# Kernel optimization log

Hardware: AMD Instinct MI355X
Metric: run time of the kernel (lower is better)

The kernel has to match this reference:

```python
import jax, jax.numpy as jnp
import numpy as np
import itertools, math

METRIC = [1.0, 1.0, 1.0]  # Cl(3,0)
EPS = 1e-6
SQRT2 = math.sqrt(2.0)


def _build_algebra(metric):
    d = len(metric)
    # basis blades ordered by grade, then lexicographic combination (repo convention)
    blades = []
    for g in range(d + 1):
        for c in itertools.combinations(range(d), g):
            blades.append(sum(1 << i for i in c))
    idx = {m: i for i, m in enumerate(blades)}
    n = len(blades)
    C = np.zeros((n, n, n), dtype=np.float32)  # cayley[i, j, k]: e_i * e_k -> sign * e_j
    for ia, am in enumerate(blades):
        for ik, bm in enumerate(blades):
            a = am >> 1
            swaps = 0
            while a:
                swaps += bin(a & bm).count('1')
                a >>= 1
            sign = -1.0 if (swaps & 1) else 1.0
            for i in range(d):
                if am & bm & (1 << i):
                    sign *= metric[i]
            C[ia, idx[am ^ bm], ik] = sign
    grades = np.array([bin(m).count('1') for m in blades])
    subspaces = np.array([int((grades == g).sum()) for g in range(d + 1)])
    paths = np.zeros((d + 1, d + 1, d + 1), dtype=bool)
    for i in range(d + 1):
        for j in range(d + 1):
            for k in range(d + 1):
                paths[i, j, k] = np.any(C[np.ix_(grades == i, grades == j, grades == k)] != 0)
    return C, subspaces, paths, grades

CAYLEY_NP, SUBSPACES, PATHS, GRADE_OF_COMP = _build_algebra(METRIC)
REP_IDX = np.repeat(np.arange(len(SUBSPACES)), SUBSPACES)  # component -> grade, len 8
PI, PJ, PK = np.nonzero(PATHS)                              # 20 active grade triples
ONEHOT_GRADE = np.eye(len(SUBSPACES), dtype=np.float32)[GRADE_OF_COMP]  # [8,4]

B, N_IN, N_OUT = 1024, 256, 256
DIM_MV = CAYLEY_NP.shape[0]  # 8
N_PATHS = int(PATHS.sum())   # 20


def mv_linear(x, w, bias=None):
    # MVLinear: per-grade weight repeated over components; einsum 'bm...i,nmi->bn...i'
    wr = w[:, :, REP_IDX]                       # [out, in, 8]
    out = jnp.einsum('bmi,nmi->bni', x, wr)
    if bias is not None:
        out = out.at[:, :, 0].add(bias[:, :, 0])  # bias embedded in scalar (grade-0) slot
    return out


def normalize_mv(x, a):
    # per-grade norms (Euclidean metric => L2 norm of each grade block)
    oh = jnp.asarray(ONEHOT_GRADE)
    norms = jnp.sqrt(jnp.einsum('bni,ig->bng', x * x, oh))  # [b, n, 4]
    interp = jax.nn.sigmoid(a)[None] * (norms - 1.0) + 1.0  # learned interp toward unit norm
    return x / (interp[:, :, REP_IDX] + EPS)


def gp_kernel(gp_weight):
    # scatter 20 path weights into (m, n, 4, 4, 4), repeat per subspace, mask by cayley
    m, n, _ = gp_weight.shape
    g = len(SUBSPACES)
    w4 = jnp.zeros((m, n, g, g, g), gp_weight.dtype).at[:, :, PI, PJ, PK].set(gp_weight)
    wrep = w4[:, :, REP_IDX][:, :, :, REP_IDX][:, :, :, :, REP_IDX]  # [m, n, 8, 8, 8]
    return jnp.asarray(CAYLEY_NP)[None, None] * wrep


def setup_inputs() -> dict:
    key = jax.random.key(0)
    ks = jax.random.split(key, 5)
    std_gp = 1.0 / math.sqrt(N_IN * (len(METRIC) + 1))
    std_lin = 1.0 / math.sqrt(N_IN)
    return {
        'x': jax.random.normal(ks[0], (B, N_IN, DIM_MV), jnp.float32),
        'w_right': jax.random.normal(ks[1], (N_IN, N_IN, len(SUBSPACES)), jnp.float32) * std_lin,
        'w_left': jax.random.normal(ks[2], (N_OUT, N_IN, len(SUBSPACES)), jnp.float32) * std_lin,
        'b_left': jax.random.normal(ks[3], (1, N_OUT, 1), jnp.float32) * 0.02,
        'norm_a': jnp.zeros((N_IN, len(SUBSPACES)), jnp.float32),  # normalization_init = 0
        'gp_weight': jax.random.normal(ks[4], (N_OUT, N_IN, N_PATHS), jnp.float32) * std_gp,
    }


def reference(x, w_right, w_left, b_left, norm_a, gp_weight):
    x_right = normalize_mv(mv_linear(x, w_right), norm_a)
    kernel = gp_kernel(gp_weight)                 # [m, n, 8, 8, 8]
    outer = jnp.einsum('bni,bnk->bnik', x, x_right)  # [b, n, 8, 8]
    prod = jnp.einsum('bnik,mnijk->bmj', outer, kernel)
    left = mv_linear(x, w_left, b_left)
    return (left + prod) / SQRT2
```

## Files before the change

### kernel.cpp

```cpp
#include <hip/hip_runtime.h>
#include <math.h>

typedef unsigned short ushortT;
typedef __bf16 bf16x8 __attribute__((ext_vector_type(8)));
typedef float  f32x4  __attribute__((ext_vector_type(4)));

__constant__ int GRADEc[8] = {0,1,1,1,2,2,2,3};

__constant__ int CMAPc[8][7] = {
  {0, 8, 9,10,11, 0, 0},
  {1,12,13,14,15,16,17},
  {2,18,19,20,21,22,23},
  {3,24,25,26,27,28,29},
  {4,30,31,32,33,34,35},
  {5,36,37,38,39,40,41},
  {6,42,43,44,45,46,47},
  {7,48,49,50,51, 0, 0}};
__constant__ int WMAPc[8][7] = {
  {0, 4, 8,14,20, 0, 0},
  {1, 5, 9,10,15,16,21},
  {1, 5, 9,10,15,16,21},
  {1, 5, 9,10,15,16,21},
  {2, 6,11,12,17,18,22},
  {2, 6,11,12,17,18,22},
  {2, 6,11,12,17,18,22},
  {3, 7,13,19,23, 0, 0}};
__constant__ int SSTARTc[8][4] = {
  {0,2,3,4},{0,2,4,6},{0,2,4,6},{0,2,4,6},
  {0,2,4,6},{0,2,4,6},{0,2,4,6},{0,2,3,4}};
__constant__ int SCOUNTc[8][4] = {
  {2,1,1,1},{2,2,2,1},{2,2,2,1},{2,2,2,1},
  {2,2,2,1},{2,2,2,1},{2,2,2,1},{2,1,1,1}};

__device__ __forceinline__ ushortT f2bf(float f) {
  unsigned int u = __float_as_uint(f);
  unsigned int r = (u + 0x7fffu + ((u >> 16) & 1u)) >> 16;
  return (ushortT)r;
}

#define GLOAD_LDS16(gsrc, ldst) \
  __builtin_amdgcn_global_load_lds((const __attribute__((address_space(1))) unsigned int*)(gsrc), \
                                   (__attribute__((address_space(3))) unsigned int*)(ldst), 16, 0, 0)

__global__ void k_xsplit(const float* __restrict__ x, ushortT* __restrict__ XH,
                         ushortT* __restrict__ XL) {
  const int b = blockIdx.x;
  const int m = threadIdx.x;
  const float4* xp = (const float4*)(x + b * 2048 + m * 8);
  float4 a = xp[0], c = xp[1];
  float v[8] = {a.x, a.y, a.z, a.w, c.x, c.y, c.z, c.w};
  #pragma unroll
  for (int i = 0; i < 8; ++i) {
    ushortT h = f2bf(v[i]);
    float hf = __uint_as_float(((unsigned int)h) << 16);
    XH[i * 262144 + b * 256 + m] = h;
    XL[i * 262144 + b * 256 + m] = f2bf(v[i] - hf);
  }
}

__global__ void k_wsplit(const float* __restrict__ w_right, ushortT* __restrict__ WH,
                         ushortT* __restrict__ WL) {
  const int n = blockIdx.x;
  const int m = threadIdx.x;
  float4 w = *(const float4*)(w_right + n * 1024 + m * 4);
  float v[4] = {w.x, w.y, w.z, w.w};
  #pragma unroll
  for (int g = 0; g < 4; ++g) {
    ushortT h = f2bf(v[g]);
    float hf = __uint_as_float(((unsigned int)h) << 16);
    WH[g * 65536 + n * 256 + m] = h;
    WL[g * 65536 + n * 256 + m] = f2bf(v[g] - hf);
  }
}

__global__ void k_build_wt2(const float* __restrict__ w_left, const float* __restrict__ gp,
                            ushortT* __restrict__ WT2b) {
  int t = blockIdx.x * 256 + threadIdx.x;
  int n = t & 255, m = (t >> 8) & 255, w = t >> 16;
  float v;
  if (w < 4)       v = w_left[m * 1024 + n * 4 + w];
  else             v = gp[m * 5120 + n * 20 + (w - 4)];
  WT2b[t] = f2bf(v);
}

__global__ __launch_bounds__(256) void k_right_mfma(const ushortT* __restrict__ XH,
                                                    const ushortT* __restrict__ XL,
                                                    const ushortT* __restrict__ WH,
                                                    const ushortT* __restrict__ WL,
                                                    float* __restrict__ y2) {
  const int i  = blockIdx.z;
  const int g  = GRADEc[i];
  const int b0 = blockIdx.y * 64;
  const int n0 = blockIdx.x * 64;
  __shared__ __align__(16) ushortT lds[4 * 2048];
  const int t = threadIdx.x;
  const int wave = t >> 6, lane = t & 63;
  const int wb = (wave & 1) * 32, wn = (wave >> 1) * 32;
  const int lrow = lane & 15, lkg = lane >> 4;

  const ushortT* Ah = XH + i * 262144 + b0 * 256;
  const ushortT* Al = XL + i * 262144 + b0 * 256;
  const ushortT* Bh = WH + g * 65536 + n0 * 256;
  const ushortT* Bl = WL + g * 65536 + n0 * 256;
  const ushortT* gp0 = (wave == 0) ? Ah : (wave == 1) ? Al : (wave == 2) ? Bh : Bl;
  ushortT* lbase = lds + wave * 2048;

  const int srow = lane >> 2;
  const int sseg = lane & 3;

  f32x4 acc[2][2];
  #pragma unroll
  for (int r = 0; r < 2; ++r)
    #pragma unroll
    for (int c = 0; c < 2; ++c)
      acc[r][c] = (f32x4){0.f, 0.f, 0.f, 0.f};

  for (int k0 = 0; k0 < 256; k0 += 32) {
    #pragma unroll
    for (int q = 0; q < 4; ++q) {
      int row = q * 16 + srow;
      int slog = sseg ^ ((row >> 1) & 3);
      GLOAD_LDS16(gp0 + row * 256 + k0 + slog * 8, lbase + q * 512);
    }
    __syncthreads();
    bf16x8 afh[2], afl[2], bfh[2], bfl[2];
    #pragma unroll
    for (int r = 0; r < 2; ++r) {
      int row = wb + r * 16 + lrow;
      int po = row * 32 + (lkg ^ ((row >> 1) & 3)) * 8;
      afh[r] = *(const bf16x8*)(lds + po);
      afl[r] = *(const bf16x8*)(lds + 2048 + po);
    }
    #pragma unroll
    for (int c = 0; c < 2; ++c) {
      int row = wn + c * 16 + lrow;
      int po = row * 32 + (lkg ^ ((row >> 1) & 3)) * 8;
      bfh[c] = *(const bf16x8*)(lds + 4096 + po);
      bfl[c] = *(const bf16x8*)(lds + 6144 + po);
    }
    #pragma unroll
    for (int r = 0; r < 2; ++r)
      #pragma unroll
      for (int c = 0; c < 2; ++c) {
        acc[r][c] = __builtin_amdgcn_mfma_f32_16x16x32_bf16(afh[r], bfh[c], acc[r][c], 0, 0, 0);
        acc[r][c] = __builtin_amdgcn_mfma_f32_16x16x32_bf16(afl[r], bfh[c], acc[r][c], 0, 0, 0);
        acc[r][c] = __builtin_amdgcn_mfma_f32_16x16x32_bf16(afh[r], bfl[c], acc[r][c], 0, 0, 0);
      }
    __syncthreads();
  }

  #pragma unroll
  for (int r = 0; r < 2; ++r)
    #pragma unroll
    for (int c = 0; c < 2; ++c)
      #pragma unroll
      for (int e = 0; e < 4; ++e) {
        int brow = b0 + wb + r * 16 + lkg * 4 + e;
        int ncol = n0 + wn + c * 16 + lrow;
        y2[i * 262144 + brow * 256 + ncol] = acc[r][c][e];
      }
}

__global__ void k_features2(const float* __restrict__ y2, const float* __restrict__ x,
                            const float* __restrict__ norm_a, ushortT* __restrict__ FT2b) {
  const int b = blockIdx.x;
  const int n = threadIdx.x;
  float y[8], xv[8];
  #pragma unroll
  for (int i = 0; i < 8; ++i) y[i] = y2[i * 262144 + b * 256 + n];
  const float4* xp = (const float4*)(x + b * 2048 + n * 8);
  float4 x01 = xp[0], x23 = xp[1];
  xv[0]=x01.x; xv[1]=x01.y; xv[2]=x01.z; xv[3]=x01.w;
  xv[4]=x23.x; xv[5]=x23.y; xv[6]=x23.z; xv[7]=x23.w;
  float4 na = *(const float4*)(norm_a + n * 4);
  float nav[4] = {na.x, na.y, na.z, na.w};
  float nr[4];
  nr[0] = fabsf(y[0]);
  nr[1] = sqrtf(y[1]*y[1] + y[2]*y[2] + y[3]*y[3]);
  nr[2] = sqrtf(y[4]*y[4] + y[5]*y[5] + y[6]*y[6]);
  nr[3] = fabsf(y[7]);
  float inv[4];
  #pragma unroll
  for (int g = 0; g < 4; ++g) {
    float s = 1.0f / (1.0f + expf(-nav[g]));
    inv[g] = 1.0f / (s * (nr[g] - 1.0f) + 1.0f + 1e-6f);
  }
  float r[8];
  r[0] = y[0]*inv[0];
  r[1] = y[1]*inv[1]; r[2] = y[2]*inv[1]; r[3] = y[3]*inv[1];
  r[4] = y[4]*inv[2]; r[5] = y[5]*inv[2]; r[6] = y[6]*inv[2];
  r[7] = y[7]*inv[3];

  float F[52];
  F[8]  = xv[0]*r[0];
  F[9]  = xv[1]*r[1] + xv[2]*r[2] + xv[3]*r[3];
  F[10] = -(xv[4]*r[4] + xv[5]*r[5] + xv[6]*r[6]);
  F[11] = -xv[7]*r[7];
  F[12] = xv[0]*r[1];
  F[13] = xv[1]*r[0];
  F[14] = -(xv[2]*r[4] + xv[3]*r[5]);
  F[15] = xv[4]*r[2] + xv[5]*r[3];
  F[16] = -xv[6]*r[7];
  F[17] = -xv[7]*r[6];
  F[18] = xv[0]*r[2];
  F[19] = xv[2]*r[0];
  F[20] = xv[1]*r[4] - xv[3]*r[6];
  F[21] = -xv[4]*r[1] + xv[6]*r[3];
  F[22] = xv[5]*r[7];
  F[23] = xv[7]*r[5];
  F[24] = xv[0]*r[3];
  F[25] = xv[3]*r[0];
  F[26] = xv[1]*r[5] + xv[2]*r[6];
  F[27] = -(xv[5]*r[1] + xv[6]*r[2]);
  F[28] = -xv[4]*r[7];
  F[29] = -xv[7]*r[4];
  F[30] = xv[0]*r[4];
  F[31] = xv[1]*r[2] - xv[2]*r[1];
  F[32] = xv[3]*r[7];
  F[33] = xv[4]*r[0];
  F[34] = -xv[5]*r[6] + xv[6]*r[5];
  F[35] = xv[7]*r[3];
  F[36] = xv[0]*r[5];
  F[37] = xv[1]*r[3] - xv[3]*r[1];
  F[38] = -xv[2]*r[7];
  F[39] = xv[5]*r[0];
  F[40] = xv[4]*r[6] - xv[6]*r[4];
  F[41] = -xv[7]*r[2];
  F[42] = xv[0]*r[6];
  F[43] = xv[2]*r[3] - xv[3]*r[2];
  F[44] = xv[1]*r[7];
  F[45] = xv[6]*r[0];
  F[46] = -xv[4]*r[5] + xv[5]*r[4];
  F[47] = xv[7]*r[1];
  F[48] = xv[0]*r[7];
  F[49] = xv[1]*r[6] - xv[2]*r[5] + xv[3]*r[4];
  F[50] = xv[4]*r[3] - xv[5]*r[2] + xv[6]*r[1];
  F[51] = xv[7]*r[0];

  #pragma unroll
  for (int c = 8; c < 52; ++c)
    FT2b[c * 262144 + b * 256 + n] = f2bf(F[c]);
}

__global__ __launch_bounds__(256) void k_gemm_mfma(const ushortT* __restrict__ XH,
                                                   const ushortT* __restrict__ FT2b,
                                                   const ushortT* __restrict__ WT2b,
                                                   float* __restrict__ outP) {
  const int j  = blockIdx.z >> 2;
  const int ks = blockIdx.z & 3;
  const int b0 = blockIdx.y * 128;
  const int m0 = blockIdx.x * 128;
  __shared__ __align__(16) ushortT sA[128 * 64];
  __shared__ __align__(16) ushortT sB[128 * 64];
  const int t    = threadIdx.x;
  const int wave = t >> 6;
  const int lane = t & 63;
  const int wb   = (wave & 1) * 64;
  const int wm   = (wave >> 1) * 64;
  const int lrow = lane & 15;
  const int lkg  = lane >> 4;
  const int srow = lane >> 3;
  const int sseg = lane & 7;

  f32x4 acc[4][4];
  #pragma unroll
  for (int r = 0; r < 4; ++r)
    #pragma unroll
    for (int c = 0; c < 4; ++c)
      acc[r][c] = (f32x4){0.f, 0.f, 0.f, 0.f};

  const int sstart = SSTARTc[j][ks];
  const int scnt   = SCOUNTc[j][ks];
  for (int s2 = 0; s2 < scnt; ++s2) {
    const int slot = sstart + s2;
    const ushortT* Ap = ((slot == 0) ? (XH + j * 262144)
                                     : (FT2b + CMAPc[j][slot] * 262144)) + b0 * 256;
    const ushortT* Bp = WT2b + WMAPc[j][slot] * 65536 + m0 * 256;
    for (int k0 = 0; k0 < 256; k0 += 64) {
      #pragma unroll
      for (int q = 0; q < 4; ++q) {
        int idx = wave * 4 + q;
        int row = idx * 8 + srow;
        int slog = sseg ^ (row & 7);
        GLOAD_LDS16(Ap + row * 256 + k0 + slog * 8, sA + idx * 512);
        GLOAD_LDS16(Bp + row * 256 + k0 + slog * 8, sB + idx * 512);
      }
      __syncthreads();
      #pragma unroll
      for (int kk = 0; kk < 2; ++kk) {
        bf16x8 af[4], bf[4];
        #pragma unroll
        for (int r = 0; r < 4; ++r) {
          int row = wb + r * 16 + lrow;
          af[r] = *(const bf16x8*)(sA + row * 64 + (((kk * 4 + lkg) ^ (row & 7)) * 8));
        }
        #pragma unroll
        for (int c = 0; c < 4; ++c) {
          int row = wm + c * 16 + lrow;
          bf[c] = *(const bf16x8*)(sB + row * 64 + (((kk * 4 + lkg) ^ (row & 7)) * 8));
        }
        #pragma unroll
        for (int r = 0; r < 4; ++r)
          #pragma unroll
          for (int c = 0; c < 4; ++c)
            acc[r][c] = __builtin_amdgcn_mfma_f32_16x16x32_bf16(af[r], bf[c], acc[r][c], 0, 0, 0);
      }
      __syncthreads();
    }
  }

  float* oj = outP + (ks * 8 + j) * 262144;
  #pragma unroll
  for (int r = 0; r < 4; ++r) {
    #pragma unroll
    for (int c = 0; c < 4; ++c) {
      #pragma unroll
      for (int e = 0; e < 4; ++e) {
        int brow = b0 + wb + r * 16 + lkg * 4 + e;
        int mcol = m0 + wm + c * 16 + lrow;
        oj[brow * 256 + mcol] = acc[r][c][e];
      }
    }
  }
}

__global__ void k_merge(const float* __restrict__ outP, const float* __restrict__ bleft,
                        float* __restrict__ out) {
  const int idx = blockIdx.x * 256 + threadIdx.x;
  const int m = idx & 255;
  const float bias = bleft[m];
  const float sc = 0.7071067811865475f;
  float o[8];
  #pragma unroll
  for (int jj = 0; jj < 8; ++jj) {
    float s = 0.0f;
    #pragma unroll
    for (int p = 0; p < 4; ++p)
      s += outP[(p * 8 + jj) * 262144 + idx];
    o[jj] = s;
  }
  o[0] += bias;
  float4 v0 = make_float4(o[0]*sc, o[1]*sc, o[2]*sc, o[3]*sc);
  float4 v1 = make_float4(o[4]*sc, o[5]*sc, o[6]*sc, o[7]*sc);
  *(float4*)(out + idx * 8)     = v0;
  *(float4*)(out + idx * 8 + 4) = v1;
}

extern "C" void kernel_launch(void* const* d_in, const int* in_sizes, int n_in,
                              void* d_out, int out_size, void* d_ws, size_t ws_size,
                              hipStream_t stream) {
  const float* x       = (const float*)d_in[0];
  const float* w_right = (const float*)d_in[1];
  const float* w_left  = (const float*)d_in[2];
  const float* b_left  = (const float*)d_in[3];
  const float* norm_a  = (const float*)d_in[4];
  const float* gp      = (const float*)d_in[5];
  float* out = (float*)d_out;
  float* W   = (float*)d_ws;

  float*   y2   = W;
  float*   outP = W + 2097152;
  ushortT* XH   = (ushortT*)(W + 10485760);
  ushortT* XL   = (ushortT*)(W + 11534336);
  ushortT* WH   = (ushortT*)(W + 12582912);
  ushortT* WL   = (ushortT*)(W + 12713984);
  ushortT* FT2b = (ushortT*)(W + 12845056);
  ushortT* WT2b = (ushortT*)(W + 19660800);

  k_xsplit<<<1024, 256, 0, stream>>>(x, XH, XL);
  k_wsplit<<<256, 256, 0, stream>>>(w_right, WH, WL);
  k_build_wt2<<<6144, 256, 0, stream>>>(w_left, gp, WT2b);
  k_right_mfma<<<dim3(4, 16, 8), 256, 0, stream>>>(XH, XL, WH, WL, y2);
  k_features2<<<1024, 256, 0, stream>>>(y2, x, norm_a, FT2b);
  k_gemm_mfma<<<dim3(2, 8, 32), 256, 0, stream>>>(XH, FT2b, WT2b, outP);
  k_merge<<<1024, 256, 0, stream>>>(outP, b_left, out);
}
```

Baseline: 121.0 us.

## Fuse prep kernels, fuse right GEMM with features, double-buffer GEMM loads

The three conversion kernels are merged into one launch. The right-side bf16x3 GEMM and the feature construction are fused through LDS, which removes the y2 round trip to global memory. Both MFMA GEMMs now double-buffer LDS so global-to-LDS loads overlap the MFMA work. The merge kernel is vectorised with float4 loads. Together these cut launch count and memory traffic, at the cost of more LDS per block and smaller 32x32 tiles in the fused kernel, which may lower occupancy or increase redundant B loads.

```diff
diff --git a/kernel.cpp b/kernel.cpp
--- a/kernel.cpp
+++ b/kernel.cpp
@@ -42,72 +42,68 @@
   __builtin_amdgcn_global_load_lds((const __attribute__((address_space(1))) unsigned int*)(gsrc), \
                                    (__attribute__((address_space(3))) unsigned int*)(ldst), 16, 0, 0)
 
-__global__ void k_xsplit(const float* __restrict__ x, ushortT* __restrict__ XH,
-                         ushortT* __restrict__ XL) {
-  const int b = blockIdx.x;
-  const int m = threadIdx.x;
-  const float4* xp = (const float4*)(x + b * 2048 + m * 8);
-  float4 a = xp[0], c = xp[1];
-  float v[8] = {a.x, a.y, a.z, a.w, c.x, c.y, c.z, c.w};
-  #pragma unroll
-  for (int i = 0; i < 8; ++i) {
-    ushortT h = f2bf(v[i]);
-    float hf = __uint_as_float(((unsigned int)h) << 16);
-    XH[i * 262144 + b * 256 + m] = h;
-    XL[i * 262144 + b * 256 + m] = f2bf(v[i] - hf);
-  }
-}
-
-__global__ void k_wsplit(const float* __restrict__ w_right, ushortT* __restrict__ WH,
-                         ushortT* __restrict__ WL) {
-  const int n = blockIdx.x;
-  const int m = threadIdx.x;
-  float4 w = *(const float4*)(w_right + n * 1024 + m * 4);
-  float v[4] = {w.x, w.y, w.z, w.w};
-  #pragma unroll
-  for (int g = 0; g < 4; ++g) {
-    ushortT h = f2bf(v[g]);
-    float hf = __uint_as_float(((unsigned int)h) << 16);
-    WH[g * 65536 + n * 256 + m] = h;
-    WL[g * 65536 + n * 256 + m] = f2bf(v[g] - hf);
-  }
-}
-
-__global__ void k_build_wt2(const float* __restrict__ w_left, const float* __restrict__ gp,
-                            ushortT* __restrict__ WT2b) {
-  int t = blockIdx.x * 256 + threadIdx.x;
-  int n = t & 255, m = (t >> 8) & 255, w = t >> 16;
-  float v;
-  if (w < 4)       v = w_left[m * 1024 + n * 4 + w];
-  else             v = gp[m * 5120 + n * 20 + (w - 4)];
-  WT2b[t] = f2bf(v);
-}
-
-__global__ __launch_bounds__(256) void k_right_mfma(const ushortT* __restrict__ XH,
+__global__ void k_prep(const float* __restrict__ x, const float* __restrict__ w_right,
+                       const float* __restrict__ w_left, const float* __restrict__ gp,
+                       ushortT* __restrict__ XH, ushortT* __restrict__ XL,
+                       ushortT* __restrict__ WH, ushortT* __restrict__ WL,
+                       ushortT* __restrict__ WT2b) {
+  const int bid = blockIdx.x;
+  const int tid = threadIdx.x;
+  if (bid < 6144) {
+    int t = bid * 256 + tid;
+    int n = t & 255, m = (t >> 8) & 255, w = t >> 16;
+    float v = (w < 4) ? w_left[m * 1024 + n * 4 + w] : gp[m * 5120 + n * 20 + (w - 4)];
+    WT2b[t] = f2bf(v);
+  } else if (bid < 7168) {
+    int b = bid - 6144;
+    const float4* xp = (const float4*)(x + b * 2048 + tid * 8);
+    float4 a = xp[0], c = xp[1];
+    float v[8] = {a.x, a.y, a.z, a.w, c.x, c.y, c.z, c.w};
+    #pragma unroll
+    for (int i = 0; i < 8; ++i) {
+      ushortT h = f2bf(v[i]);
+      float hf = __uint_as_float(((unsigned int)h) << 16);
+      XH[i * 262144 + b * 256 + tid] = h;
+      XL[i * 262144 + b * 256 + tid] = f2bf(v[i] - hf);
+    }
+  } else {
+    int n = bid - 7168;
+    float4 w = *(const float4*)(w_right + n * 1024 + tid * 4);
+    float v[4] = {w.x, w.y, w.z, w.w};
+    #pragma unroll
+    for (int g = 0; g < 4; ++g) {
+      ushortT h = f2bf(v[g]);
+      float hf = __uint_as_float(((unsigned int)h) << 16);
+      WH[g * 65536 + n * 256 + tid] = h;
+      WL[g * 65536 + n * 256 + tid] = f2bf(v[g] - hf);
+    }
+  }
+}
+
+__global__ __launch_bounds__(512) void k_right_feat(const ushortT* __restrict__ XH,
                                                     const ushortT* __restrict__ XL,
                                                     const ushortT* __restrict__ WH,
                                                     const ushortT* __restrict__ WL,
-                                                    float* __restrict__ y2) {
-  const int i  = blockIdx.z;
-  const int g  = GRADEc[i];
-  const int b0 = blockIdx.y * 64;
-  const int n0 = blockIdx.x * 64;
-  __shared__ __align__(16) ushortT lds[4 * 2048];
-  const int t = threadIdx.x;
-  const int wave = t >> 6, lane = t & 63;
-  const int wb = (wave & 1) * 32, wn = (wave >> 1) * 32;
+                                                    const float* __restrict__ x,
+                                                    const float* __restrict__ norm_a,
+                                                    ushortT* __restrict__ FT2b) {
+  const int n0 = blockIdx.x * 32;
+  const int b0 = blockIdx.y * 32;
+  __shared__ __align__(16) ushortT lds[49152];
+  const int t    = threadIdx.x;
+  const int wave = t >> 6;
+  const int lane = t & 63;
+  const int i    = wave;
+  const int g    = GRADEc[i];
   const int lrow = lane & 15, lkg = lane >> 4;
-
-  const ushortT* Ah = XH + i * 262144 + b0 * 256;
-  const ushortT* Al = XL + i * 262144 + b0 * 256;
-  const ushortT* Bh = WH + g * 65536 + n0 * 256;
-  const ushortT* Bl = WL + g * 65536 + n0 * 256;
-  const ushortT* gp0 = (wave == 0) ? Ah : (wave == 1) ? Al : (wave == 2) ? Bh : Bl;
-  ushortT* lbase = lds + wave * 2048;
-
   const int srow = lane >> 2;
   const int sseg = lane & 3;
 
+  const ushortT* Asrc_h = XH + i * 262144 + b0 * 256;
+  const ushortT* Asrc_l = XL + i * 262144 + b0 * 256;
+  const int bg = wave >> 1;
+  const ushortT* Bsrc = ((wave & 1) ? WL : WH) + bg * 65536 + n0 * 256;
+
   f32x4 acc[2][2];
   #pragma unroll
   for (int r = 0; r < 2; ++r)
@@ -115,28 +111,35 @@
     for (int c = 0; c < 2; ++c)
       acc[r][c] = (f32x4){0.f, 0.f, 0.f, 0.f};
 
-  for (int k0 = 0; k0 < 256; k0 += 32) {
-    #pragma unroll
-    for (int q = 0; q < 4; ++q) {
+  auto STAGE = [&](int k0, int buf) {
+    ushortT* base = lds + buf * 24576;
+    #pragma unroll
+    for (int q = 0; q < 2; ++q) {
       int row = q * 16 + srow;
       int slog = sseg ^ ((row >> 1) & 3);
-      GLOAD_LDS16(gp0 + row * 256 + k0 + slog * 8, lbase + q * 512);
-    }
-    __syncthreads();
+      GLOAD_LDS16(Asrc_h + row * 256 + k0 + slog * 8, base + i * 1024 + q * 512);
+      GLOAD_LDS16(Asrc_l + row * 256 + k0 + slog * 8, base + 8192 + i * 1024 + q * 512);
+      GLOAD_LDS16(Bsrc   + row * 256 + k0 + slog * 8,
+                  base + 16384 + (wave & 1) * 4096 + bg * 1024 + q * 512);
+    }
+  };
+
+  auto COMPUTE = [&](int buf) {
+    const ushortT* base = lds + buf * 24576;
     bf16x8 afh[2], afl[2], bfh[2], bfl[2];
     #pragma unroll
     for (int r = 0; r < 2; ++r) {
-      int row = wb + r * 16 + lrow;
+      int row = r * 16 + lrow;
       int po = row * 32 + (lkg ^ ((row >> 1) & 3)) * 8;
-      afh[r] = *(const bf16x8*)(lds + po);
-      afl[r] = *(const bf16x8*)(lds + 2048 + po);
+      afh[r] = *(const bf16x8*)(base + i * 1024 + po);
+      afl[r] = *(const bf16x8*)(base + 8192 + i * 1024 + po);
     }
     #pragma unroll
     for (int c = 0; c < 2; ++c) {
-      int row = wn + c * 16 + lrow;
+      int row = c * 16 + lrow;
       int po = row * 32 + (lkg ^ ((row >> 1) & 3)) * 8;
-      bfh[c] = *(const bf16x8*)(lds + 4096 + po);
-      bfl[c] = *(const bf16x8*)(lds + 6144 + po);
+      bfh[c] = *(const bf16x8*)(base + 16384 + g * 1024 + po);
+      bfl[c] = *(const bf16x8*)(base + 20480 + g * 1024 + po);
     }
     #pragma unroll
     for (int r = 0; r < 2; ++r)
@@ -146,100 +149,111 @@
         acc[r][c] = __builtin_amdgcn_mfma_f32_16x16x32_bf16(afl[r], bfh[c], acc[r][c], 0, 0, 0);
         acc[r][c] = __builtin_amdgcn_mfma_f32_16x16x32_bf16(afh[r], bfl[c], acc[r][c], 0, 0, 0);
       }
+  };
+
+  STAGE(0, 0);
+  __syncthreads();
+  int cur = 0;
+  for (int tc = 0; tc < 8; ++tc) {
+    if (tc < 7) STAGE((tc + 1) * 32, cur ^ 1);
+    COMPUTE(cur);
     __syncthreads();
-  }
-
+    cur ^= 1;
+  }
+
+  float* yl = (float*)lds;
   #pragma unroll
   for (int r = 0; r < 2; ++r)
     #pragma unroll
     for (int c = 0; c < 2; ++c)
       #pragma unroll
       for (int e = 0; e < 4; ++e) {
-        int brow = b0 + wb + r * 16 + lkg * 4 + e;
-        int ncol = n0 + wn + c * 16 + lrow;
-        y2[i * 262144 + brow * 256 + ncol] = acc[r][c][e];
+        int row = r * 16 + lkg * 4 + e;
+        int col = c * 16 + lrow;
+        yl[i * 1056 + row * 33 + col] = acc[r][c][e];
       }
-}
-
-__global__ void k_features2(const float* __restrict__ y2, const float* __restrict__ x,
-                            const float* __restrict__ norm_a, ushortT* __restrict__ FT2b) {
-  const int b = blockIdx.x;
-  const int n = threadIdx.x;
-  float y[8], xv[8];
-  #pragma unroll
-  for (int i = 0; i < 8; ++i) y[i] = y2[i * 262144 + b * 256 + n];
-  const float4* xp = (const float4*)(x + b * 2048 + n * 8);
-  float4 x01 = xp[0], x23 = xp[1];
-  xv[0]=x01.x; xv[1]=x01.y; xv[2]=x01.z; xv[3]=x01.w;
-  xv[4]=x23.x; xv[5]=x23.y; xv[6]=x23.z; xv[7]=x23.w;
-  float4 na = *(const float4*)(norm_a + n * 4);
-  float nav[4] = {na.x, na.y, na.z, na.w};
-  float nr[4];
-  nr[0] = fabsf(y[0]);
-  nr[1] = sqrtf(y[1]*y[1] + y[2]*y[2] + y[3]*y[3]);
-  nr[2] = sqrtf(y[4]*y[4] + y[5]*y[5] + y[6]*y[6]);
-  nr[3] = fabsf(y[7]);
-  float inv[4];
-  #pragma unroll
-  for (int g = 0; g < 4; ++g) {
-    float s = 1.0f / (1.0f + expf(-nav[g]));
-    inv[g] = 1.0f / (s * (nr[g] - 1.0f) + 1.0f + 1e-6f);
-  }
-  float r[8];
-  r[0] = y[0]*inv[0];
-  r[1] = y[1]*inv[1]; r[2] = y[2]*inv[1]; r[3] = y[3]*inv[1];
-  r[4] = y[4]*inv[2]; r[5] = y[5]*inv[2]; r[6] = y[6]*inv[2];
-  r[7] = y[7]*inv[3];
-
-  float F[52];
-  F[8]  = xv[0]*r[0];
-  F[9]  = xv[1]*r[1] + xv[2]*r[2] + xv[3]*r[3];
-  F[10] = -(xv[4]*r[4] + xv[5]*r[5] + xv[6]*r[6]);
-  F[11] = -xv[7]*r[7];
-  F[12] = xv[0]*r[1];
-  F[13] = xv[1]*r[0];
-  F[14] = -(xv[2]*r[4] + xv[3]*r[5]);
-  F[15] = xv[4]*r[2] + xv[5]*r[3];
-  F[16] = -xv[6]*r[7];
-  F[17] = -xv[7]*r[6];
-  F[18] = xv[0]*r[2];
-  F[19] = xv[2]*r[0];
-  F[20] = xv[1]*r[4] - xv[3]*r[6];
-  F[21] = -xv[4]*r[1] + xv[6]*r[3];
-  F[22] = xv[5]*r[7];
-  F[23] = xv[7]*r[5];
-  F[24] = xv[0]*r[3];
-  F[25] = xv[3]*r[0];
-  F[26] = xv[1]*r[5] + xv[2]*r[6];
-  F[27] = -(xv[5]*r[1] + xv[6]*r[2]);
-  F[28] = -xv[4]*r[7];
-  F[29] = -xv[7]*r[4];
-  F[30] = xv[0]*r[4];
-  F[31] = xv[1]*r[2] - xv[2]*r[1];
-  F[32] = xv[3]*r[7];
-  F[33] = xv[4]*r[0];
-  F[34] = -xv[5]*r[6] + xv[6]*r[5];
-  F[35] = xv[7]*r[3];
-  F[36] = xv[0]*r[5];
-  F[37] = xv[1]*r[3] - xv[3]*r[1];
-  F[38] = -xv[2]*r[7];
-  F[39] = xv[5]*r[0];
-  F[40] = xv[4]*r[6] - xv[6]*r[4];
-  F[41] = -xv[7]*r[2];
-  F[42] = xv[0]*r[6];
-  F[43] = xv[2]*r[3] - xv[3]*r[2];
-  F[44] = xv[1]*r[7];
-  F[45] = xv[6]*r[0];
-  F[46] = -xv[4]*r[5] + xv[5]*r[4];
-  F[47] = xv[7]*r[1];
-  F[48] = xv[0]*r[7];
-  F[49] = xv[1]*r[6] - xv[2]*r[5] + xv[3]*r[4];
-  F[50] = xv[4]*r[3] - xv[5]*r[2] + xv[6]*r[1];
-  F[51] = xv[7]*r[0];
-
-  #pragma unroll
-  for (int c = 8; c < 52; ++c)
-    FT2b[c * 262144 + b * 256 + n] = f2bf(F[c]);
+  __syncthreads();
+
+  #pragma unroll
+  for (int e2 = 0; e2 < 2; ++e2) {
+    int el  = t + e2 * 512;
+    int row = el >> 5, col = el & 31;
+    int b = b0 + row, n = n0 + col;
+    float y[8];
+    #pragma unroll
+    for (int q = 0; q < 8; ++q) y[q] = yl[q * 1056 + row * 33 + col];
+    const float4* xp = (const float4*)(x + b * 2048 + n * 8);
+    float4 x01 = xp[0], x23 = xp[1];
+    float xv[8] = {x01.x, x01.y, x01.z, x01.w, x23.x, x23.y, x23.z, x23.w};
+    float4 na = *(const float4*)(norm_a + n * 4);
+    float nav[4] = {na.x, na.y, na.z, na.w};
+    float nr[4];
+    nr[0] = fabsf(y[0]);
+    nr[1] = sqrtf(y[1]*y[1] + y[2]*y[2] + y[3]*y[3]);
+    nr[2] = sqrtf(y[4]*y[4] + y[5]*y[5] + y[6]*y[6]);
+    nr[3] = fabsf(y[7]);
+    float inv[4];
+    #pragma unroll
+    for (int gg = 0; gg < 4; ++gg) {
+      float s = 1.0f / (1.0f + expf(-nav[gg]));
+      inv[gg] = 1.0f / (s * (nr[gg] - 1.0f) + 1.0f + 1e-6f);
+    }
+    float r[8];
+    r[0] = y[0]*inv[0];
+    r[1] = y[1]*inv[1]; r[2] = y[2]*inv[1]; r[3] = y[3]*inv[1];
+    r[4] = y[4]*inv[2]; r[5] = y[5]*inv[2]; r[6] = y[6]*inv[2];
+    r[7] = y[7]*inv[3];
+
+    float F[52];
+    F[8]  = xv[0]*r[0];
+    F[9]  = xv[1]*r[1] + xv[2]*r[2] + xv[3]*r[3];
+    F[10] = -(xv[4]*r[4] + xv[5]*r[5] + xv[6]*r[6]);
+    F[11] = -xv[7]*r[7];
+    F[12] = xv[0]*r[1];
+    F[13] = xv[1]*r[0];
+    F[14] = -(xv[2]*r[4] + xv[3]*r[5]);
+    F[15] = xv[4]*r[2] + xv[5]*r[3];
+    F[16] = -xv[6]*r[7];
+    F[17] = -xv[7]*r[6];
+    F[18] = xv[0]*r[2];
+    F[19] = xv[2]*r[0];
+    F[20] = xv[1]*r[4] - xv[3]*r[6];
+    F[21] = -xv[4]*r[1] + xv[6]*r[3];
+    F[22] = xv[5]*r[7];
+    F[23] = xv[7]*r[5];
+    F[24] = xv[0]*r[3];
+    F[25] = xv[3]*r[0];
+    F[26] = xv[1]*r[5] + xv[2]*r[6];
+    F[27] = -(xv[5]*r[1] + xv[6]*r[2]);
+    F[28] = -xv[4]*r[7];
+    F[29] = -xv[7]*r[4];
+    F[30] = xv[0]*r[4];
+    F[31] = xv[1]*r[2] - xv[2]*r[1];
+    F[32] = xv[3]*r[7];
+    F[33] = xv[4]*r[0];
+    F[34] = -xv[5]*r[6] + xv[6]*r[5];
+    F[35] = xv[7]*r[3];
+    F[36] = xv[0]*r[5];
+    F[37] = xv[1]*r[3] - xv[3]*r[1];
+    F[38] = -xv[2]*r[7];
+    F[39] = xv[5]*r[0];
+    F[40] = xv[4]*r[6] - xv[6]*r[4];
+    F[41] = -xv[7]*r[2];
+    F[42] = xv[0]*r[6];
+    F[43] = xv[2]*r[3] - xv[3]*r[2];
+    F[44] = xv[1]*r[7];
+    F[45] = xv[6]*r[0];
+    F[46] = -xv[4]*r[5] + xv[5]*r[4];
+    F[47] = xv[7]*r[1];
+    F[48] = xv[0]*r[7];
+    F[49] = xv[1]*r[6] - xv[2]*r[5] + xv[3]*r[4];
+    F[50] = xv[4]*r[3] - xv[5]*r[2] + xv[6]*r[1];
+    F[51] = xv[7]*r[0];
+
+    #pragma unroll
+    for (int c = 8; c < 52; ++c)
+      FT2b[c * 262144 + b * 256 + n] = f2bf(F[c]);
+  }
 }
 
 __global__ __launch_bounds__(256) void k_gemm_mfma(const ushortT* __restrict__ XH,
@@ -250,8 +264,7 @@
   const int ks = blockIdx.z & 3;
   const int b0 = blockIdx.y * 128;
   const int m0 = blockIdx.x * 128;
-  __shared__ __align__(16) ushortT sA[128 * 64];
-  __shared__ __align__(16) ushortT sB[128 * 64];
+  __shared__ __align__(16) ushortT lds[32768];
   const int t    = threadIdx.x;
   const int wave = t >> 6;
   const int lane = t & 63;
@@ -270,43 +283,52 @@
       acc[r][c] = (f32x4){0.f, 0.f, 0.f, 0.f};
 
   const int sstart = SSTARTc[j][ks];
-  const int scnt   = SCOUNTc[j][ks];
-  for (int s2 = 0; s2 < scnt; ++s2) {
-    const int slot = sstart + s2;
+  const int nt     = SCOUNTc[j][ks] * 4;
+
+  auto STAGE = [&](int tch, int buf) {
+    int slot = sstart + (tch >> 2);
+    int k0   = (tch & 3) << 6;
     const ushortT* Ap = ((slot == 0) ? (XH + j * 262144)
                                      : (FT2b + CMAPc[j][slot] * 262144)) + b0 * 256;
     const ushortT* Bp = WT2b + WMAPc[j][slot] * 65536 + m0 * 256;
-    for (int k0 = 0; k0 < 256; k0 += 64) {
-      #pragma unroll
-      for (int q = 0; q < 4; ++q) {
-        int idx = wave * 4 + q;
-        int row = idx * 8 + srow;
-        int slog = sseg ^ (row & 7);
-        GLOAD_LDS16(Ap + row * 256 + k0 + slog * 8, sA + idx * 512);
-        GLOAD_LDS16(Bp + row * 256 + k0 + slog * 8, sB + idx * 512);
+    #pragma unroll
+    for (int q = 0; q < 4; ++q) {
+      int idx = wave * 4 + q;
+      int row = idx * 8 + srow;
+      int slog = sseg ^ (row & 7);
+      GLOAD_LDS16(Ap + row * 256 + k0 + slog * 8, lds + buf * 8192 + idx * 512);
+      GLOAD_LDS16(Bp + row * 256 + k0 + slog * 8, lds + 16384 + buf * 8192 + idx * 512);
+    }
+  };
+
+  STAGE(0, 0);
+  __syncthreads();
+  int cur = 0;
+  for (int tc = 0; tc < nt; ++tc) {
+    if (tc + 1 < nt) STAGE(tc + 1, cur ^ 1);
+    const ushortT* sA = lds + cur * 8192;
+    const ushortT* sB = lds + 16384 + cur * 8192;
+    #pragma unroll
+    for (int kk = 0; kk < 2; ++kk) {
+      bf16x8 af[4], bf[4];
+      #pragma unroll
+      for (int r = 0; r < 4; ++r) {
+        int row = wb + r * 16 + lrow;
+        af[r] = *(const bf16x8*)(sA + row * 64 + (((kk * 4 + lkg) ^ (row & 7)) * 8));
       }
-      __syncthreads();
-      #pragma unroll
-      for (int kk = 0; kk < 2; ++kk) {
-        bf16x8 af[4], bf[4];
+      #pragma unroll
+      for (int c = 0; c < 4; ++c) {
+        int row = wm + c * 16 + lrow;
+        bf[c] = *(const bf16x8*)(sB + row * 64 + (((kk * 4 + lkg) ^ (row & 7)) * 8));
+      }
+      #pragma unroll
+      for (int r = 0; r < 4; ++r)
         #pragma unroll
-        for (int r = 0; r < 4; ++r) {
-          int row = wb + r * 16 + lrow;
-          af[r] = *(const bf16x8*)(sA + row * 64 + (((kk * 4 + lkg) ^ (row & 7)) * 8));
-        }
-        #pragma unroll
-        for (int c = 0; c < 4; ++c) {
-          int row = wm + c * 16 + lrow;
-          bf[c] = *(const bf16x8*)(sB + row * 64 + (((kk * 4 + lkg) ^ (row & 7)) * 8));
-        }
-        #pragma unroll
-        for (int r = 0; r < 4; ++r)
-          #pragma unroll
-          for (int c = 0; c < 4; ++c)
-            acc[r][c] = __builtin_amdgcn_mfma_f32_16x16x32_bf16(af[r], bf[c], acc[r][c], 0, 0, 0);
-      }
-      __syncthreads();
-    }
+        for (int c = 0; c < 4; ++c)
+          acc[r][c] = __builtin_amdgcn_mfma_f32_16x16x32_bf16(af[r], bf[c], acc[r][c], 0, 0, 0);
+    }
+    __syncthreads();
+    cur ^= 1;
   }
 
   float* oj = outP + (ks * 8 + j) * 262144;
@@ -326,24 +348,31 @@
 
 __global__ void k_merge(const float* __restrict__ outP, const float* __restrict__ bleft,
                         float* __restrict__ out) {
-  const int idx = blockIdx.x * 256 + threadIdx.x;
-  const int m = idx & 255;
-  const float bias = bleft[m];
+  const int t4 = (blockIdx.x * 256 + threadIdx.x) * 4;
+  const int m  = t4 & 255;
   const float sc = 0.7071067811865475f;
-  float o[8];
+  float o[4][8];
   #pragma unroll
   for (int jj = 0; jj < 8; ++jj) {
-    float s = 0.0f;
-    #pragma unroll
-    for (int p = 0; p < 4; ++p)
-      s += outP[(p * 8 + jj) * 262144 + idx];
-    o[jj] = s;
-  }
-  o[0] += bias;
-  float4 v0 = make_float4(o[0]*sc, o[1]*sc, o[2]*sc, o[3]*sc);
-  float4 v1 = make_float4(o[4]*sc, o[5]*sc, o[6]*sc, o[7]*sc);
-  *(float4*)(out + idx * 8)     = v0;
-  *(float4*)(out + idx * 8 + 4) = v1;
+    float4 s = make_float4(0.f, 0.f, 0.f, 0.f);
+    #pragma unroll
+    for (int p = 0; p < 4; ++p) {
+      float4 v = *(const float4*)(outP + (p * 8 + jj) * 262144 + t4);
+      s.x += v.x; s.y += v.y; s.z += v.z; s.w += v.w;
+    }
+    o[0][jj] = s.x; o[1][jj] = s.y; o[2][jj] = s.z; o[3][jj] = s.w;
+  }
+  #pragma unroll
+  for (int q = 0; q < 4; ++q) {
+    float ov[8];
+    #pragma unroll
+    for (int jj = 0; jj < 8; ++jj) ov[jj] = o[q][jj];
+    ov[0] += bleft[m + q];
+    float4 v0 = make_float4(ov[0]*sc, ov[1]*sc, ov[2]*sc, ov[3]*sc);
+    float4 v1 = make_float4(ov[4]*sc, ov[5]*sc, ov[6]*sc, ov[7]*sc);
+    *(float4*)(out + (t4 + q) * 8)     = v0;
+    *(float4*)(out + (t4 + q) * 8 + 4) = v1;
+  }
 }
 
 extern "C" void kernel_launch(void* const* d_in, const int* in_sizes, int n_in,
@@ -358,20 +387,16 @@
   float* out = (float*)d_out;
   float* W   = (float*)d_ws;
 
-  float*   y2   = W;
-  float*   outP = W + 2097152;
-  ushortT* XH   = (ushortT*)(W + 10485760);
-  ushortT* XL   = (ushortT*)(W + 11534336);
-  ushortT* WH   = (ushortT*)(W + 12582912);
-  ushortT* WL   = (ushortT*)(W + 12713984);
-  ushortT* FT2b = (ushortT*)(W + 12845056);
-  ushortT* WT2b = (ushortT*)(W + 19660800);
-
-  k_xsplit<<<1024, 256, 0, stream>>>(x, XH, XL);
-  k_wsplit<<<256, 256, 0, stream>>>(w_right, WH, WL);
-  k_build_wt2<<<6144, 256, 0, stream>>>(w_left, gp, WT2b);
-  k_right_mfma<<<dim3(4, 16, 8), 256, 0, stream>>>(XH, XL, WH, WL, y2);
-  k_features2<<<1024, 256, 0, stream>>>(y2, x, norm_a, FT2b);
+  float*   outP = W;
+  ushortT* XH   = (ushortT*)(W + 8388608);
+  ushortT* XL   = (ushortT*)(W + 9437184);
+  ushortT* WH   = (ushortT*)(W + 10485760);
+  ushortT* WL   = (ushortT*)(W + 10616832);
+  ushortT* FT2b = (ushortT*)(W + 10747904);
+  ushortT* WT2b = (ushortT*)(W + 17563648);
+
+  k_prep<<<7424, 256, 0, stream>>>(x, w_right, w_left, gp, XH, XL, WH, WL, WT2b);
+  k_right_feat<<<dim3(8, 32), 512, 0, stream>>>(XH, XL, WH, WL, x, norm_a, FT2b);
   k_gemm_mfma<<<dim3(2, 8, 32), 256, 0, stream>>>(XH, FT2b, WT2b, outP);
-  k_merge<<<1024, 256, 0, stream>>>(outP, b_left, out);
-}
+  k_merge<<<256, 256, 0, stream>>>(outP, b_left, out);
+}
```

New measurement: 123.2 us. About the same (+1.9%).
